# Kernel tuning notes

Hardware: AMD Instinct MI355X
Metric: run time of the kernel (lower is better)

The kernel has to match this reference:

```python
import jax, jax.numpy as jnp
import numpy as np

VOCAB, EMB, HID, OUT, T, B = 50000, 512, 1024, 1, 256, 256


def setup_inputs() -> dict:
    key = jax.random.key(0)
    ks = jax.random.split(key, 8)
    s_ih = 1.0 / np.sqrt(HID)
    return {
        "text": jax.random.randint(ks[0], (B, T), 0, VOCAB, dtype=jnp.int64),
        "emb": jax.random.normal(ks[1], (VOCAB, EMB), jnp.float32),
        "w_ih": jax.random.uniform(ks[2], (4 * HID, EMB), jnp.float32, -s_ih, s_ih),
        "w_hh": jax.random.uniform(ks[3], (4 * HID, HID), jnp.float32, -s_ih, s_ih),
        "b_ih": jax.random.uniform(ks[4], (4 * HID,), jnp.float32, -s_ih, s_ih),
        "b_hh": jax.random.uniform(ks[5], (4 * HID,), jnp.float32, -s_ih, s_ih),
        "fc_w": jax.random.uniform(ks[6], (OUT, HID), jnp.float32, -s_ih, s_ih),
        "fc_b": jax.random.uniform(ks[7], (OUT,), jnp.float32, -s_ih, s_ih),
    }


def _lstm_last_hidden(x, w_ih, w_hh, b_ih, b_hh):
    # x: [B, T, E]. Precompute input contribution to all gates: [B, T, 4H].
    xg = jnp.einsum("bte,ge->btg", x, w_ih) + b_ih + b_hh
    Bn = x.shape[0]
    H = w_hh.shape[1]
    h0 = jnp.zeros((Bn, H), x.dtype)
    c0 = jnp.zeros((Bn, H), x.dtype)

    def step(carry, xt):
        h, c = carry
        gates = xt + h @ w_hh.T  # [B, 4H], PyTorch gate order i,f,g,o
        i, f, g, o = jnp.split(gates, 4, axis=-1)
        c = jax.nn.sigmoid(f) * c + jax.nn.sigmoid(i) * jnp.tanh(g)
        h = jax.nn.sigmoid(o) * jnp.tanh(c)
        return (h, c), None

    (h, c), _ = jax.lax.scan(step, (h0, c0), jnp.swapaxes(xg, 0, 1))
    return h  # last hidden state [B, H]


def reference(text, emb, w_ih, w_hh, b_ih, b_hh, fc_w, fc_b):
    x = emb[text]  # [B, T, E]
    h = _lstm_last_hidden(x, w_ih, w_hh, b_ih, b_hh)
    return jax.nn.sigmoid(h @ fc_w.T + fc_b)  # [B, OUT]
```

## Files before the change

kernel.cpp:

```cpp
#include <hip/hip_runtime.h>

#define TT 256
#define BB 256
#define EE 512
#define HH 1024
#define G4 4096
#define KTOT 1536
#define BK 128
#define APAD 8

typedef __attribute__((ext_vector_type(8))) short short8;
typedef __attribute__((ext_vector_type(4))) float f32x4;

__device__ __forceinline__ short f2bf(float f) {
    unsigned u; __builtin_memcpy(&u, &f, 4);
    unsigned r = (u + 0x7FFFu + ((u >> 16) & 1u)) >> 16;
    return (short)(unsigned short)r;
}
__device__ __forceinline__ float bf2f(short s) {
    unsigned u = ((unsigned)(unsigned short)s) << 16;
    float f; __builtin_memcpy(&f, &u, 4);
    return f;
}
__device__ __forceinline__ float sigf(float x) { return 1.f / (1.f + __expf(-x)); }

__global__ __launch_bounds__(256) void prep_kernel(
    const float* __restrict__ w_ih, const float* __restrict__ w_hh,
    const float* __restrict__ b_ih, const float* __restrict__ b_hh,
    short* __restrict__ w_cat, float* __restrict__ bias)
{
    int r = blockIdx.x;
    int tid = threadIdx.x;
    for (int c = tid; c < KTOT; c += 256) {
        float v = (c < HH) ? w_hh[(size_t)r * HH + c]
                           : w_ih[(size_t)r * EE + (c - HH)];
        w_cat[(size_t)r * KTOT + c] = f2bf(v);
    }
    if (tid == 0) bias[r] = b_ih[r] + b_hh[r];
}

__global__ __launch_bounds__(256) void gather_kernel(
    const int* __restrict__ text, const float* __restrict__ emb,
    short* __restrict__ xbf)
{
    int row = blockIdx.x * 4 + (threadIdx.x >> 6);
    int b = row >> 8, t = row & 255;
    int lane = threadIdx.x & 63;
    int v = text[row];
    const float* src = emb + (size_t)v * EE + lane * 8;
    float4 f0 = *(const float4*)src;
    float4 f1 = *(const float4*)(src + 4);
    float fv[8];
    *(float4*)&fv[0] = f0; *(float4*)&fv[4] = f1;
    short8 s;
    #pragma unroll
    for (int i = 0; i < 8; ++i) s[i] = f2bf(fv[i]);
    *(short8*)(xbf + ((size_t)t * BB + b) * EE + lane * 8) = s;
}

__global__ __launch_bounds__(256) void lstm_step(
    const short* __restrict__ w_cat,
    const float* __restrict__ bias,
    const short* __restrict__ xbf,
    const short* __restrict__ h_in,
    short*       __restrict__ h_out,
    float*       __restrict__ c_st,
    int t)
{
    __shared__ short At[2][64][BK + APAD];
    __shared__ float Gt[4][64][17];

    const int tid  = threadIdx.x;
    const int wv   = tid >> 6;
    const int lane = tid & 63;
    const int n    = lane & 15;
    const int q    = lane >> 4;

    const int bid = blockIdx.x;
    const int xcd = bid & 7, sub = bid >> 3;
    const int j0  = (xcd * 8 + (sub & 7)) * 16;
    const int b0  = (sub >> 3) * 64;

    const short* wrow = w_cat + (size_t)(wv * HH + j0 + n) * KTOT;

    const int ar = tid >> 2;
    const int ac = (tid & 3) * 32;
    const int ab = b0 + ar;
    const short* hrow = h_in + (size_t)ab * HH;
    const short* xrow = xbf + ((size_t)t * BB + ab) * EE - HH;

    const int kstart = (t == 0) ? HH : 0;
    const int niter  = (KTOT - kstart) / BK;

    f32x4 acc[4];
    #pragma unroll
    for (int i = 0; i < 4; ++i) acc[i] = (f32x4){0.f, 0.f, 0.f, 0.f};

    {
        const short* s = ((kstart < HH) ? hrow : xrow) + kstart + ac;
        *(short8*)&At[0][ar][ac]      = *(const short8*)(s);
        *(short8*)&At[0][ar][ac + 8]  = *(const short8*)(s + 8);
        *(short8*)&At[0][ar][ac + 16] = *(const short8*)(s + 16);
        *(short8*)&At[0][ar][ac + 24] = *(const short8*)(s + 24);
    }
    __syncthreads();

    for (int i = 0; i < niter; ++i) {
        const int k0  = kstart + i * BK;
        const int cur = i & 1;
        const bool more = (i + 1 < niter);
        short8 r0, r1, r2, r3;
        if (more) {
            const int kn = k0 + BK;
            const short* s = ((kn < HH) ? hrow : xrow) + kn + ac;
            r0 = *(const short8*)(s);
            r1 = *(const short8*)(s + 8);
            r2 = *(const short8*)(s + 16);
            r3 = *(const short8*)(s + 24);
        }
        #pragma unroll
        for (int ks = 0; ks < 4; ++ks) {
            short8 bfrag = *(const short8*)(wrow + k0 + ks * 32 + q * 8);
            #pragma unroll
            for (int mt = 0; mt < 4; ++mt) {
                short8 afrag = *(const short8*)&At[cur][mt * 16 + n][ks * 32 + q * 8];
                acc[mt] = __builtin_amdgcn_mfma_f32_16x16x32_bf16(afrag, bfrag, acc[mt], 0, 0, 0);
            }
        }
        if (more) {
            *(short8*)&At[cur ^ 1][ar][ac]      = r0;
            *(short8*)&At[cur ^ 1][ar][ac + 8]  = r1;
            *(short8*)&At[cur ^ 1][ar][ac + 16] = r2;
            *(short8*)&At[cur ^ 1][ar][ac + 24] = r3;
            __syncthreads();
        }
    }

    #pragma unroll
    for (int mt = 0; mt < 4; ++mt)
        #pragma unroll
        for (int r = 0; r < 4; ++r)
            Gt[wv][mt * 16 + q * 4 + r][n] = acc[mt][r];
    __syncthreads();

    const int m  = tid >> 2;
    const int n4 = (tid & 3) * 4;
    const int b  = b0 + m;
    #pragma unroll
    for (int u = 0; u < 4; ++u) {
        const int nn = n4 + u;
        const int j  = j0 + nn;
        float ip = Gt[0][m][nn] + bias[j];
        float fp = Gt[1][m][nn] + bias[HH + j];
        float gp = Gt[2][m][nn] + bias[2 * HH + j];
        float op = Gt[3][m][nn] + bias[3 * HH + j];
        float co = (t == 0) ? 0.f : c_st[(size_t)b * HH + j];
        float cn = sigf(fp) * co + sigf(ip) * tanhf(gp);
        float hn = sigf(op) * tanhf(cn);
        c_st[(size_t)b * HH + j] = cn;
        h_out[(size_t)b * HH + j] = f2bf(hn);
    }
}

__global__ __launch_bounds__(256) void fc_kernel(
    const short* __restrict__ hbuf, const float* __restrict__ fc_w,
    const float* __restrict__ fc_b, float* __restrict__ out)
{
    __shared__ float red[4];
    int b = blockIdx.x;
    int tid = threadIdx.x;
    float s = 0.f;
    for (int k = tid; k < HH; k += 256)
        s += bf2f(hbuf[(size_t)b * HH + k]) * fc_w[k];
    #pragma unroll
    for (int off = 32; off > 0; off >>= 1) s += __shfl_down(s, off);
    if ((tid & 63) == 0) red[tid >> 6] = s;
    __syncthreads();
    if (tid == 0) {
        float tot = red[0] + red[1] + red[2] + red[3] + fc_b[0];
        out[b] = 1.f / (1.f + __expf(-tot));
    }
}

extern "C" void kernel_launch(void* const* d_in, const int* in_sizes, int n_in,
                              void* d_out, int out_size, void* d_ws, size_t ws_size,
                              hipStream_t stream) {
    const int*   text = (const int*)d_in[0];
    const float* emb  = (const float*)d_in[1];
    const float* w_ih = (const float*)d_in[2];
    const float* w_hh = (const float*)d_in[3];
    const float* b_ih = (const float*)d_in[4];
    const float* b_hh = (const float*)d_in[5];
    const float* fc_w = (const float*)d_in[6];
    const float* fc_b = (const float*)d_in[7];
    float* out = (float*)d_out;

    char* ws = (char*)d_ws;
    short* w_cat = (short*)(ws);
    float* bias  = (float*)(ws + 12582912);
    short* xbf   = (short*)(ws + 12599296);
    short* hbuf0 = (short*)(ws + 79708160);
    short* hbuf1 = (short*)(ws + 80232448);
    float* c_st  = (float*)(ws + 80756736);

    gather_kernel<<<dim3(BB * TT / 4), dim3(256), 0, stream>>>(text, emb, xbf);
    prep_kernel<<<dim3(G4), dim3(256), 0, stream>>>(w_ih, w_hh, b_ih, b_hh, w_cat, bias);

    for (int t = 0; t < TT; ++t) {
        const short* hin  = (t & 1) ? hbuf1 : hbuf0;
        short*       hout = (t & 1) ? hbuf0 : hbuf1;
        lstm_step<<<dim3(256), dim3(256), 0, stream>>>(
            w_cat, bias, xbf, hin, hout, c_st, t);
    }

    fc_kernel<<<dim3(BB), dim3(256), 0, stream>>>(hbuf0, fc_w, fc_b, out);
}
```

Baseline: 4.906 ms.

## Replace per-timestep launches with persistent LSTM kernel using a grid barrier

The 256 per-step kernel launches become one persistent kernel of 256 blocks with 1024 threads. Each block loads its W_hh slice into LDS once, keeps the cell state in registers and synchronises all blocks after each step with an atomic-counter barrier. The aim is to remove per-step launch overhead, repeated weight reads from global/L2 and the c-state memory traffic. In exchange it relies on all 256 blocks being co-resident, one per CU using roughly 149KB of LDS, and it adds spin-barrier latency every step.

```diff
diff --git a/kernel.cpp b/kernel.cpp
--- a/kernel.cpp
+++ b/kernel.cpp
@@ -6,8 +6,7 @@
 #define HH 1024
 #define G4 4096
 #define KTOT 1536
-#define BK 128
-#define APAD 8
+#define NBLK 256
 
 typedef __attribute__((ext_vector_type(8))) short short8;
 typedef __attribute__((ext_vector_type(4))) float f32x4;
@@ -58,21 +57,22 @@
     *(short8*)(xbf + ((size_t)t * BB + b) * EE + lane * 8) = s;
 }
 
-__global__ __launch_bounds__(256) void lstm_step(
+__global__ __launch_bounds__(1024, 4) void lstm_persist(
     const short* __restrict__ w_cat,
     const float* __restrict__ bias,
     const short* __restrict__ xbf,
-    const short* __restrict__ h_in,
-    short*       __restrict__ h_out,
-    float*       __restrict__ c_st,
-    int t)
-{
-    __shared__ short At[2][64][BK + APAD];
+    short* __restrict__ hbuf0,
+    short* __restrict__ hbuf1,
+    unsigned* __restrict__ bar)
+{
+    __shared__ short Wl[64][1032];
     __shared__ float Gt[4][64][17];
 
     const int tid  = threadIdx.x;
     const int wv   = tid >> 6;
     const int lane = tid & 63;
+    const int g    = wv & 3;
+    const int mt   = wv >> 2;
     const int n    = lane & 15;
     const int q    = lane >> 4;
 
@@ -81,84 +81,78 @@
     const int j0  = (xcd * 8 + (sub & 7)) * 16;
     const int b0  = (sub >> 3) * 64;
 
-    const short* wrow = w_cat + (size_t)(wv * HH + j0 + n) * KTOT;
-
-    const int ar = tid >> 2;
-    const int ac = (tid & 3) * 32;
-    const int ab = b0 + ar;
-    const short* hrow = h_in + (size_t)ab * HH;
-    const short* xrow = xbf + ((size_t)t * BB + ab) * EE - HH;
-
-    const int kstart = (t == 0) ? HH : 0;
-    const int niter  = (KTOT - kstart) / BK;
-
-    f32x4 acc[4];
-    #pragma unroll
-    for (int i = 0; i < 4; ++i) acc[i] = (f32x4){0.f, 0.f, 0.f, 0.f};
-
-    {
-        const short* s = ((kstart < HH) ? hrow : xrow) + kstart + ac;
-        *(short8*)&At[0][ar][ac]      = *(const short8*)(s);
-        *(short8*)&At[0][ar][ac + 8]  = *(const short8*)(s + 8);
-        *(short8*)&At[0][ar][ac + 16] = *(const short8*)(s + 16);
-        *(short8*)&At[0][ar][ac + 24] = *(const short8*)(s + 24);
-    }
+    for (int i = tid; i < 64 * 128; i += 1024) {
+        int row = i >> 7, ch = i & 127;
+        int gg = row >> 4, nn = row & 15;
+        *(short8*)&Wl[row][ch * 8] =
+            *(const short8*)(w_cat + (size_t)(gg * HH + j0 + nn) * KTOT + ch * 8);
+    }
+
+    const int em = tid >> 4;
+    const int en = tid & 15;
+    float creg = 0.f;
+    const float b_i = bias[j0 + en];
+    const float b_f = bias[HH + j0 + en];
+    const float b_g = bias[2 * HH + j0 + en];
+    const float b_o = bias[3 * HH + j0 + en];
+
+    const short* wrow_x = w_cat + (size_t)(g * HH + j0 + n) * KTOT + HH;
+    short* hO = hbuf0 + (size_t)(b0 + em) * HH + j0 + en;
+    short* hE = hbuf1 + (size_t)(b0 + em) * HH + j0 + en;
+
     __syncthreads();
 
-    for (int i = 0; i < niter; ++i) {
-        const int k0  = kstart + i * BK;
-        const int cur = i & 1;
-        const bool more = (i + 1 < niter);
-        short8 r0, r1, r2, r3;
-        if (more) {
-            const int kn = k0 + BK;
-            const short* s = ((kn < HH) ? hrow : xrow) + kn + ac;
-            r0 = *(const short8*)(s);
-            r1 = *(const short8*)(s + 8);
-            r2 = *(const short8*)(s + 16);
-            r3 = *(const short8*)(s + 24);
-        }
-        #pragma unroll
-        for (int ks = 0; ks < 4; ++ks) {
-            short8 bfrag = *(const short8*)(wrow + k0 + ks * 32 + q * 8);
-            #pragma unroll
-            for (int mt = 0; mt < 4; ++mt) {
-                short8 afrag = *(const short8*)&At[cur][mt * 16 + n][ks * 32 + q * 8];
-                acc[mt] = __builtin_amdgcn_mfma_f32_16x16x32_bf16(afrag, bfrag, acc[mt], 0, 0, 0);
+    for (int t = 0; t < TT; ++t) {
+        const short* hin = (t & 1) ? hbuf1 : hbuf0;
+
+        f32x4 acc = (f32x4){0.f, 0.f, 0.f, 0.f};
+        const short* arow_h = hin + (size_t)(b0 + mt * 16 + n) * HH + q * 8;
+        const short* arow_x = xbf + ((size_t)t * BB + b0 + mt * 16 + n) * EE + q * 8;
+        const short* Wrow   = &Wl[g * 16 + n][q * 8];
+
+        if (t > 0) {
+            #pragma unroll 4
+            for (int kc = 0; kc < 32; ++kc) {
+                short8 af = *(const short8*)(arow_h + kc * 32);
+                short8 bf = *(const short8*)(Wrow + kc * 32);
+                acc = __builtin_amdgcn_mfma_f32_16x16x32_bf16(af, bf, acc, 0, 0, 0);
             }
         }
-        if (more) {
-            *(short8*)&At[cur ^ 1][ar][ac]      = r0;
-            *(short8*)&At[cur ^ 1][ar][ac + 8]  = r1;
-            *(short8*)&At[cur ^ 1][ar][ac + 16] = r2;
-            *(short8*)&At[cur ^ 1][ar][ac + 24] = r3;
-            __syncthreads();
+        #pragma unroll 4
+        for (int kc = 0; kc < 16; ++kc) {
+            short8 af = *(const short8*)(arow_x + kc * 32);
+            short8 bf = *(const short8*)(wrow_x + q * 8 + kc * 32);
+            acc = __builtin_amdgcn_mfma_f32_16x16x32_bf16(af, bf, acc, 0, 0, 0);
         }
-    }
-
-    #pragma unroll
-    for (int mt = 0; mt < 4; ++mt)
-        #pragma unroll
-        for (int r = 0; r < 4; ++r)
-            Gt[wv][mt * 16 + q * 4 + r][n] = acc[mt][r];
-    __syncthreads();
-
-    const int m  = tid >> 2;
-    const int n4 = (tid & 3) * 4;
-    const int b  = b0 + m;
-    #pragma unroll
-    for (int u = 0; u < 4; ++u) {
-        const int nn = n4 + u;
-        const int j  = j0 + nn;
-        float ip = Gt[0][m][nn] + bias[j];
-        float fp = Gt[1][m][nn] + bias[HH + j];
-        float gp = Gt[2][m][nn] + bias[2 * HH + j];
-        float op = Gt[3][m][nn] + bias[3 * HH + j];
-        float co = (t == 0) ? 0.f : c_st[(size_t)b * HH + j];
-        float cn = sigf(fp) * co + sigf(ip) * tanhf(gp);
+
+        const int gm = mt * 16 + q * 4;
+        Gt[g][gm + 0][n] = acc[0];
+        Gt[g][gm + 1][n] = acc[1];
+        Gt[g][gm + 2][n] = acc[2];
+        Gt[g][gm + 3][n] = acc[3];
+        __syncthreads();
+
+        float ip = Gt[0][em][en] + b_i;
+        float fp = Gt[1][em][en] + b_f;
+        float gp = Gt[2][em][en] + b_g;
+        float op = Gt[3][em][en] + b_o;
+        float cn = sigf(fp) * creg + sigf(ip) * tanhf(gp);
+        creg = cn;
         float hn = sigf(op) * tanhf(cn);
-        c_st[(size_t)b * HH + j] = cn;
-        h_out[(size_t)b * HH + j] = f2bf(hn);
+        *((t & 1) ? hO : hE) = f2bf(hn);
+
+        __syncthreads();
+        if (tid == 0) {
+            __threadfence();
+            __hip_atomic_fetch_add(bar, 1u, __ATOMIC_RELEASE, __HIP_MEMORY_SCOPE_AGENT);
+            const unsigned target = (unsigned)NBLK * (unsigned)(t + 1);
+            long guard = 0;
+            while (__hip_atomic_load(bar, __ATOMIC_ACQUIRE, __HIP_MEMORY_SCOPE_AGENT) < target) {
+                __builtin_amdgcn_s_sleep(1);
+                if (++guard > (1L << 40)) break;
+            }
+        }
+        __syncthreads();
     }
 }
 
@@ -196,22 +190,19 @@
     float* out = (float*)d_out;
 
     char* ws = (char*)d_ws;
-    short* w_cat = (short*)(ws);
-    float* bias  = (float*)(ws + 12582912);
-    short* xbf   = (short*)(ws + 12599296);
-    short* hbuf0 = (short*)(ws + 79708160);
-    short* hbuf1 = (short*)(ws + 80232448);
-    float* c_st  = (float*)(ws + 80756736);
-
+    short*    w_cat = (short*)(ws);
+    float*    bias  = (float*)(ws + 12582912);
+    short*    xbf   = (short*)(ws + 12599296);
+    short*    hbuf0 = (short*)(ws + 79708160);
+    short*    hbuf1 = (short*)(ws + 80232448);
+    unsigned* bar   = (unsigned*)(ws + 80756736);
+
+    hipMemsetAsync(bar, 0, 64, stream);
     gather_kernel<<<dim3(BB * TT / 4), dim3(256), 0, stream>>>(text, emb, xbf);
     prep_kernel<<<dim3(G4), dim3(256), 0, stream>>>(w_ih, w_hh, b_ih, b_hh, w_cat, bias);
 
-    for (int t = 0; t < TT; ++t) {
-        const short* hin  = (t & 1) ? hbuf1 : hbuf0;
-        short*       hout = (t & 1) ? hbuf0 : hbuf1;
-        lstm_step<<<dim3(256), dim3(256), 0, stream>>>(
-            w_cat, bias, xbf, hin, hout, c_st, t);
-    }
+    lstm_persist<<<dim3(NBLK), dim3(1024), 0, stream>>>(
+        w_cat, bias, xbf, hbuf0, hbuf1, bar);
 
     fc_kernel<<<dim3(BB), dim3(256), 0, stream>>>(hbuf0, fc_w, fc_b, out);
 }
```

New measurement: 12.75 ms. +159.9%, slower.
